# Kernel tuning notes

Hardware: AMD Instinct MI355X
Metric: run time of the kernel (lower is better)

Reference implementation:

```python
import jax, jax.numpy as jnp
import numpy as np

BATCH, D_IN, D_FEAT, DEGREE = 16384, 1024, 4096, 3


def setup_inputs() -> dict:
    key = jax.random.key(0)
    kx, kw = jax.random.split(key)
    x = jax.random.normal(kx, (BATCH, D_IN), dtype=jnp.float32)
    W = jax.random.normal(kw, (DEGREE, D_IN, D_FEAT), dtype=jnp.float32)
    log_lengthscale = jnp.zeros((1,), dtype=jnp.float32)  # lengthscale = 1
    log_var = jnp.zeros((1,), dtype=jnp.float32)          # var = 1
    return {"x": x, "W": W, "log_lengthscale": log_lengthscale, "log_var": log_var}


def reference(x, W, log_lengthscale, log_var):
    # x: [B, d_in], W: [degree, d_in, d_feat]
    inv_ls = jnp.exp(-log_lengthscale)          # scalar lengthscale (ard=False)
    xs = x * inv_ls                             # x / exp(log_lengthscale)
    # degree independent gaussian projections: [degree, B, d_feat]
    proj = jnp.einsum('bi,kio->kbo', xs, W)
    # elementwise product over the degree axis (sequential multiply in torch)
    sketch = jnp.prod(proj, axis=0)             # [B, d_feat]
    inv_sqrt_d = jnp.float32(1.0 / np.sqrt(D_FEAT))
    return sketch * inv_sqrt_d * jnp.exp(0.5 * log_var)
```

## Files before the change

### kernel.cpp

```cpp
#include <hip/hip_runtime.h>


#define BATCH 16384
#define DIN   1024
#define DFEAT 4096

typedef short short8 __attribute__((ext_vector_type(8)));
typedef float f32x4  __attribute__((ext_vector_type(4)));
typedef unsigned short ushort8v __attribute__((ext_vector_type(8)));

__device__ __forceinline__ unsigned short f2bf(float f) {
  unsigned int u = __float_as_uint(f);
  u += 0x7FFFu + ((u >> 16) & 1u);
  return (unsigned short)(u >> 16);
}

__global__ void cast_x_kernel(const float4* __restrict__ x,
                              const float* __restrict__ log_ls,
                              ushort8v* __restrict__ xs) {
  float inv = expf(-log_ls[0]);
  int i = blockIdx.x * 256 + threadIdx.x;
  float4 v0 = x[i * 2];
  float4 v1 = x[i * 2 + 1];
  ushort8v o;
  o[0] = f2bf(v0.x * inv); o[1] = f2bf(v0.y * inv);
  o[2] = f2bf(v0.z * inv); o[3] = f2bf(v0.w * inv);
  o[4] = f2bf(v1.x * inv); o[5] = f2bf(v1.y * inv);
  o[6] = f2bf(v1.z * inv); o[7] = f2bf(v1.w * inv);
  xs[i] = o;
}

__global__ void transpose_w_kernel(const float* __restrict__ W,
                                   unsigned short* __restrict__ Wt) {
  __shared__ float tile[32][65];
  int d  = blockIdx.z;
  int i0 = blockIdx.y * 32;
  int o0 = blockIdx.x * 64;
  int tid = threadIdx.x;
  const float* src = W + (size_t)d * DIN * DFEAT + (size_t)i0 * DFEAT + o0;
  #pragma unroll
  for (int j = 0; j < 2; ++j) {
    int idx = j * 256 + tid;
    int r = idx >> 4;
    int c = (idx & 15) * 4;
    float4 v = *(const float4*)(src + (size_t)r * DFEAT + c);
    tile[r][c + 0] = v.x; tile[r][c + 1] = v.y;
    tile[r][c + 2] = v.z; tile[r][c + 3] = v.w;
  }
  __syncthreads();
  unsigned short* dst = Wt + (size_t)d * DFEAT * DIN + (size_t)o0 * DIN + i0;
  #pragma unroll
  for (int j = 0; j < 2; ++j) {
    int idx = j * 256 + tid;
    int r = idx >> 3;
    int c = (idx & 7) * 4;
    ushort4 u;
    u.x = f2bf(tile[c + 0][r]);
    u.y = f2bf(tile[c + 1][r]);
    u.z = f2bf(tile[c + 2][r]);
    u.w = f2bf(tile[c + 3][r]);
    *(ushort4*)(dst + (size_t)r * DIN + c) = u;
  }
}

__global__ __launch_bounds__(256, 2) void sketch_gemm_kernel(
    const unsigned short* __restrict__ xs,
    const unsigned short* __restrict__ Wt,
    const float* __restrict__ log_var,
    float* __restrict__ out) {
  __shared__ unsigned short As[2][128 * 64];
  __shared__ unsigned short Bs[2][3][64 * 64];

  const int tid  = threadIdx.x;
  const int lane = tid & 63;
  const int w    = tid >> 6;
  const int wm   = w >> 1;
  const int wn   = w & 1;
  const int row  = lane & 15;
  const int quad = lane >> 4;

  int bid = blockIdx.x;
  int xcd = bid & 7;
  int t0  = bid >> 3;
  int bn  = (xcd << 3) + (t0 & 7);
  int bm  = t0 >> 3;

  f32x4 acc[3][4][2];
  #pragma unroll
  for (int d = 0; d < 3; ++d)
    #pragma unroll
    for (int mi = 0; mi < 4; ++mi)
      #pragma unroll
      for (int ni = 0; ni < 2; ++ni)
        acc[d][mi][ni] = (f32x4){0.f, 0.f, 0.f, 0.f};

  const unsigned short* xsrc = xs + (size_t)(bm * 128) * DIN;
  const unsigned short* wsrc = Wt + (size_t)(bn * 64) * DIN;

#define STAGE_A(DSTBUF, K0)                                                    \
  {                                                                            \
    _Pragma("unroll")                                                          \
    for (int j = 0; j < 4; ++j) {                                              \
      int gi = (w << 2) + j;                                                   \
      int gc = (gi << 6) + lane;                         \
      int mm = gc >> 3;                                                        \
      int cc = (gc & 7) ^ (mm & 7);                                            \
      __builtin_amdgcn_global_load_lds(                                        \
          (const __attribute__((address_space(1))) void*)(                     \
              xsrc + (size_t)mm * DIN + (K0) + cc * 8),                        \
          (__attribute__((address_space(3))) void*)(&As[DSTBUF][gi << 9]),     \
          16, 0, 0);                                                           \
    }                                                                          \
  }

#define STAGE_B(DSTBUF, MAT, K0)                                               \
  {                                                                            \
    _Pragma("unroll")                                                          \
    for (int j = 0; j < 2; ++j) {                                              \
      int gi = (w << 1) + j;                                                   \
      int gc = (gi << 6) + lane;                          \
      int nn = gc >> 3;                                                        \
      int cc = (gc & 7) ^ (nn & 7);                                            \
      __builtin_amdgcn_global_load_lds(                                        \
          (const __attribute__((address_space(1))) void*)(                     \
              wsrc + (size_t)(MAT) * (DFEAT * DIN) + (size_t)nn * DIN + (K0) + cc * 8), \
          (__attribute__((address_space(3))) void*)(&Bs[DSTBUF][MAT][gi << 9]),\
          16, 0, 0);                                                           \
    }                                                                          \
  }

#define READ_A(SRCBUF, DST)                                                    \
  _Pragma("unroll")                                                            \
  for (int mi = 0; mi < 4; ++mi) {                                             \
    _Pragma("unroll")                                                          \
    for (int kh = 0; kh < 2; ++kh) {                                           \
      int mm = wm * 64 + mi * 16 + row;                                        \
      int pp = ((kh << 2) + quad) ^ (mm & 7);                                  \
      DST[mi][kh] = *(const short8*)(&As[SRCBUF][mm * 64 + pp * 8]);           \
    }                                                                          \
  }

#define READ_B(SRCBUF, MAT, DST)                                               \
  _Pragma("unroll")                                                            \
  for (int ni = 0; ni < 2; ++ni) {                                             \
    _Pragma("unroll")                                                          \
    for (int kh = 0; kh < 2; ++kh) {                                           \
      int nn = wn * 32 + ni * 16 + row;                                        \
      int pp = ((kh << 2) + quad) ^ (nn & 7);                                  \
      DST[ni][kh] = *(const short8*)(&Bs[SRCBUF][MAT][nn * 64 + pp * 8]);      \
    }                                                                          \
  }

#define MFMA_P(MAT, AARR, BARR)                                                \
  __builtin_amdgcn_s_setprio(1);                                               \
  _Pragma("unroll")                                                            \
  for (int mi = 0; mi < 4; ++mi)                                               \
    _Pragma("unroll")                                                          \
    for (int ni = 0; ni < 2; ++ni)                                             \
      _Pragma("unroll")                                                        \
      for (int kh = 0; kh < 2; ++kh)                                           \
        acc[MAT][mi][ni] = __builtin_amdgcn_mfma_f32_16x16x32_bf16(            \
            AARR[mi][kh], BARR[ni][kh], acc[MAT][mi][ni], 0, 0, 0);            \
  __builtin_amdgcn_s_setprio(0);                                               \
  __builtin_amdgcn_sched_barrier(0);

#define ENTRY(N)                                                               \
  asm volatile("s_waitcnt vmcnt(" #N ")" ::: "memory");                        \
  __builtin_amdgcn_s_barrier();                                                \
  __builtin_amdgcn_sched_barrier(0);

#define TILE_BODY(T, AC, AA, BX, BY, CB, NB)                                   \
  {                                                                            \
    const int kn_ = ((T) + 1) << 6;                                            \
                                    \
    ENTRY(2);                                                                  \
    READ_B(CB, 1, BY);                                                         \
    STAGE_A(NB, kn_);                                                          \
    STAGE_B(NB, 0, kn_);                                                       \
    __builtin_amdgcn_sched_barrier(0);                                         \
    MFMA_P(0, AC, BX);                                                         \
                                      \
    ENTRY(6);                                                                  \
    READ_B(CB, 2, BX);                                                         \
    STAGE_B(NB, 1, kn_);                                                       \
    __builtin_amdgcn_sched_barrier(0);                                         \
    MFMA_P(1, AC, BY);                                                         \
                    \
    ENTRY(2);                                                                  \
    READ_A(NB, AA);                                                            \
    READ_B(NB, 0, BY);                                                         \
    STAGE_B(NB, 2, kn_);                                                       \
    __builtin_amdgcn_sched_barrier(0);                                         \
    MFMA_P(2, AC, BX);                                                         \
  }

  short8 a0[4][2], a1[4][2];
  short8 bx[2][2], by[2][2];

  STAGE_A(0, 0);
  STAGE_B(0, 0, 0);
  STAGE_B(0, 1, 0);
  STAGE_B(0, 2, 0);
  asm volatile("s_waitcnt vmcnt(4)" ::: "memory");
  __builtin_amdgcn_s_barrier();
  __builtin_amdgcn_sched_barrier(0);
  READ_A(0, a0);
  READ_B(0, 0, bx);

  #pragma unroll 1
  for (int i = 0; i < 7; ++i) {
    const int t = i * 2;
    TILE_BODY(t,     a0, a1, bx, by, 0, 1);
    TILE_BODY(t + 1, a1, a0, by, bx, 1, 0);
  }
  TILE_BODY(14, a0, a1, bx, by, 0, 1);

  ENTRY(2);
  READ_B(1, 1, bx);
  __builtin_amdgcn_sched_barrier(0);
  MFMA_P(0, a1, by);

  ENTRY(0);
  READ_B(1, 2, by);
  __builtin_amdgcn_sched_barrier(0);
  MFMA_P(1, a1, bx);

  MFMA_P(2, a1, by);

  float sc = 0.015625f * expf(0.5f * log_var[0]);
  #pragma unroll
  for (int mi = 0; mi < 4; ++mi) {
    #pragma unroll
    for (int ni = 0; ni < 2; ++ni) {
      int colg = bn * 64 + wn * 32 + ni * 16 + row;
      int rowg = bm * 128 + wm * 64 + mi * 16 + quad * 4;
      #pragma unroll
      for (int t2 = 0; t2 < 4; ++t2) {
        float v = acc[0][mi][ni][t2] * acc[1][mi][ni][t2] * acc[2][mi][ni][t2] * sc;
        out[(size_t)(rowg + t2) * DFEAT + colg] = v;
      }
    }
  }
#undef STAGE_A
#undef STAGE_B
#undef READ_A
#undef READ_B
#undef MFMA_P
#undef ENTRY
#undef TILE_BODY
}

extern "C" void kernel_launch(void* const* d_in, const int* in_sizes, int n_in,
                              void* d_out, int out_size, void* d_ws, size_t ws_size,
                              hipStream_t stream) {
  const float* x   = (const float*)d_in[0];
  const float* W   = (const float*)d_in[1];
  const float* lls = (const float*)d_in[2];
  const float* lv  = (const float*)d_in[3];
  float* out = (float*)d_out;

  unsigned short* xs = (unsigned short*)d_ws;
  unsigned short* Wt = xs + (size_t)BATCH * DIN;

  cast_x_kernel<<<BATCH * DIN / 8 / 256, 256, 0, stream>>>(
      (const float4*)x, lls, (ushort8v*)xs);

  transpose_w_kernel<<<dim3(DFEAT / 64, DIN / 32, 3), dim3(256), 0, stream>>>(W, Wt);

  sketch_gemm_kernel<<<(BATCH / 128) * (DFEAT / 64), 256, 0, stream>>>(xs, Wt, lv, out);
}
```

Measured before the change: 712.2 us.

## Load A fragments directly from global into registers, bypassing LDS

```diff
diff --git a/kernel.cpp b/kernel.cpp
--- a/kernel.cpp
+++ b/kernel.cpp
@@ -68,7 +68,6 @@
     const unsigned short* __restrict__ Wt,
     const float* __restrict__ log_var,
     float* __restrict__ out) {
-  __shared__ unsigned short As[2][128 * 64];
   __shared__ unsigned short Bs[2][3][64 * 64];
 
   const int tid  = threadIdx.x;
@@ -96,22 +95,7 @@
 
   const unsigned short* xsrc = xs + (size_t)(bm * 128) * DIN;
   const unsigned short* wsrc = Wt + (size_t)(bn * 64) * DIN;
-
-#define STAGE_A(DSTBUF, K0)                                                    \
-  {                                                                            \
-    _Pragma("unroll")                                                          \
-    for (int j = 0; j < 4; ++j) {                                              \
-      int gi = (w << 2) + j;                                                   \
-      int gc = (gi << 6) + lane;                         \
-      int mm = gc >> 3;                                                        \
-      int cc = (gc & 7) ^ (mm & 7);                                            \
-      __builtin_amdgcn_global_load_lds(                                        \
-          (const __attribute__((address_space(1))) void*)(                     \
-              xsrc + (size_t)mm * DIN + (K0) + cc * 8),                        \
-          (__attribute__((address_space(3))) void*)(&As[DSTBUF][gi << 9]),     \
-          16, 0, 0);                                                           \
-    }                                                                          \
-  }
+  const unsigned short* aptr = xsrc + (size_t)(wm * 64 + row) * DIN + (quad << 3);
 
 #define STAGE_B(DSTBUF, MAT, K0)                                               \
   {                                                                            \
@@ -129,14 +113,13 @@
     }                                                                          \
   }
 
-#define READ_A(SRCBUF, DST)                                                    \
+#define LOAD_A(DST, K0)                                                        \
   _Pragma("unroll")                                                            \
   for (int mi = 0; mi < 4; ++mi) {                                             \
     _Pragma("unroll")                                                          \
     for (int kh = 0; kh < 2; ++kh) {                                           \
-      int mm = wm * 64 + mi * 16 + row;                                        \
-      int pp = ((kh << 2) + quad) ^ (mm & 7);                                  \
-      DST[mi][kh] = *(const short8*)(&As[SRCBUF][mm * 64 + pp * 8]);           \
+      DST[mi][kh] = *(const short8*)(aptr + (size_t)(mi * 16) * DIN +          \
+                                     (K0) + kh * 32);                          \
     }                                                                          \
   }
 
@@ -172,22 +155,22 @@
 #define TILE_BODY(T, AC, AA, BX, BY, CB, NB)                                   \
   {                                                                            \
     const int kn_ = ((T) + 1) << 6;                                            \
-                                    \
+                         \
     ENTRY(2);                                                                  \
     READ_B(CB, 1, BY);                                                         \
-    STAGE_A(NB, kn_);                                                          \
     STAGE_B(NB, 0, kn_);                                                       \
+    __builtin_amdgcn_sched_barrier(0);          \
+    LOAD_A(AA, kn_);                                                           \
     __builtin_amdgcn_sched_barrier(0);                                         \
     MFMA_P(0, AC, BX);                                                         \
                                       \
-    ENTRY(6);                                                                  \
+    ENTRY(10);                                                                 \
     READ_B(CB, 2, BX);                                                         \
     STAGE_B(NB, 1, kn_);                                                       \
     __builtin_amdgcn_sched_barrier(0);                                         \
     MFMA_P(1, AC, BY);                                                         \
-                    \
-    ENTRY(2);                                                                  \
-    READ_A(NB, AA);                                                            \
+                            \
+    ENTRY(10);                                                                 \
     READ_B(NB, 0, BY);                                                         \
     STAGE_B(NB, 2, kn_);                                                       \
     __builtin_amdgcn_sched_barrier(0);                                         \
@@ -197,14 +180,15 @@
   short8 a0[4][2], a1[4][2];
   short8 bx[2][2], by[2][2];
 
-  STAGE_A(0, 0);
   STAGE_B(0, 0, 0);
+  __builtin_amdgcn_sched_barrier(0);
+  LOAD_A(a0, 0);
+  __builtin_amdgcn_sched_barrier(0);
   STAGE_B(0, 1, 0);
   STAGE_B(0, 2, 0);
-  asm volatile("s_waitcnt vmcnt(4)" ::: "memory");
+  asm volatile("s_waitcnt vmcnt(12)" ::: "memory");
   __builtin_amdgcn_s_barrier();
   __builtin_amdgcn_sched_barrier(0);
-  READ_A(0, a0);
   READ_B(0, 0, bx);
 
   #pragma unroll 1
@@ -241,9 +225,8 @@
       }
     }
   }
-#undef STAGE_A
 #undef STAGE_B
-#undef READ_A
+#undef LOAD_A
 #undef READ_B
 #undef MFMA_P
 #undef ENTRY
```

Result: slower. 902.3 us (+26.7%).
